# Kernel optimization log

Measured on AMD Instinct MI355X. Metric: run time of the kernel, lower is better.

Reference implementation:

```python
import jax, jax.numpy as jnp
import numpy as np

K = 3  # n_neighbors


def setup_inputs() -> dict:
    key = jax.random.key(0)
    k1, k2, k3 = jax.random.split(key, 3)
    N, D, C, B = 400000, 27, 11, 512  # train size, 3*N_PEAKS_MAX, classes, query batch
    train_features = jax.random.normal(k1, (N, D), dtype=jnp.float32)
    label_idx = jax.random.randint(k2, (N,), 0, C)
    train_labels = jax.nn.one_hot(label_idx, C, dtype=jnp.float32)
    query = jax.random.normal(k3, (B, D), dtype=jnp.float32)
    return {"query": query, "train_features": train_features, "train_labels": train_labels}


def _divide_no_nan(x, y):
    # tf.math.divide_no_nan: 0 where denominator is 0
    y_safe = jnp.where(y != 0, y, 1.0)
    return jnp.where(y != 0, x / y_safe, 0.0)


def reference(query, train_features, train_labels):
    # scale = per-feature max abs over training set (computed in __init__)
    scale = jnp.max(jnp.abs(train_features), axis=0)            # [D]
    train_s = _divide_no_nan(train_features, scale)             # [N,D]
    q_s = _divide_no_nan(query, scale)                          # [B,D]

    xn = jnp.sum(train_s * train_s, axis=1)                     # [N]
    qn = jnp.sum(q_s * q_s, axis=1)                             # [B]
    d2 = qn[:, None] - 2.0 * jnp.einsum('bd,nd->bn', q_s, train_s) + xn[None, :]
    dist = jnp.sqrt(jnp.maximum(d2, 0.0))                       # [B,N]

    neg_kd, idx = jax.lax.top_k(-dist, K)                       # k smallest distances
    kd = -neg_kd                                                # [B,K]

    lab = train_labels[idx]                                     # [B,K,C]
    # inverse-distance weighted vote (safe against zero distances)
    kd_safe = jnp.where(kd == 0.0, 1.0, kd)
    votes = jnp.sum(lab / kd_safe[:, :, None], axis=1)          # [B,C]
    vote_res = jax.nn.one_hot(jnp.argmax(votes, axis=1), train_labels.shape[1], dtype=jnp.float32)

    # exact-match branch: if the nearest distance is 0, return its label directly
    zero_hit = (jnp.min(kd, axis=1) == 0.0)[:, None]            # [B,1]
    result = jnp.where(zero_hit, lab[:, 0, :], vote_res)        # [B,C]
    return kd, result
```

## Files before the change

kernel.cpp:

```cpp
#include <hip/hip_runtime.h>
#include <math.h>

typedef _Float16 h8 __attribute__((ext_vector_type(8)));
typedef float    f4v __attribute__((ext_vector_type(4)));

#define N_TRAIN 400000
#define DIMS    27
#define BQ      512
#define NCLS    11
#define KNN     3
#define NB      500
#define P1T     1024
#define PTS_BLK 800
#define PTS_SUP 160
#define NSUP    5
#define NPT     10
#define RAWF    4320
#define TILE_B  2048
#define NC      (NB * KNN)
#define SB      1024
#define RPB     392
#define SROWS   128
#define P2T     512

#define U64MAX 0xFFFFFFFFFFFFFFFFULL

__global__ __launch_bounds__(256) void k_scale(const float* __restrict__ train,
                                               unsigned* __restrict__ scale_u) {
    __shared__ float st[SROWS * DIMS];
    __shared__ float sp[243];
    int tid = threadIdx.x;
    int r0 = blockIdx.x * RPB;
    int r1 = min(r0 + RPB, N_TRAIN);
    int c  = tid % DIMS;
    int rr = tid / DIMS;
    float m = 0.f;
    for (int base = r0; base < r1; base += SROWS) {
        int cnt = min(SROWS, r1 - base);
        int tot4 = (cnt * DIMS) >> 2;
        const uint4* src4 = (const uint4*)(train + (size_t)base * DIMS);
        uint4* st4 = (uint4*)st;
        for (int i = tid; i < tot4; i += 256) st4[i] = src4[i];
        __syncthreads();
        if (tid < 243) {
            for (int r = rr; r < cnt; r += 9)
                m = fmaxf(m, fabsf(st[r * DIMS + c]));
        }
        __syncthreads();
    }
    if (tid < 243) sp[tid] = m;
    __syncthreads();
    if (tid < DIMS) {
        float v = 0.f;
#pragma unroll
        for (int g = 0; g < 9; ++g) v = fmaxf(v, sp[g * DIMS + tid]);
        atomicMax(&scale_u[tid], __float_as_uint(v));
    }
}

__global__ __launch_bounds__(64) void k_qprep(const float* __restrict__ query,
                                              const unsigned* __restrict__ scale_u,
                                              _Float16* __restrict__ Qhi,
                                              _Float16* __restrict__ Qlo) {
    int q = blockIdx.x * 64 + threadIdx.x;
    if (q >= BQ) return;
    const float* r = query + (size_t)q * DIMS;
#pragma unroll
    for (int d = 0; d < 32; ++d) {
        _Float16 hi = (_Float16)0.f, lo = (_Float16)0.f;
        if (d < DIMS) {
            float sc = __uint_as_float(scale_u[d]);
            float inv = (sc != 0.f) ? 1.f / sc : 0.f;
            float xs = r[d] * inv;
            hi = (_Float16)xs;
            lo = (_Float16)(xs - (float)hi);
        } else if (d == 27) {
            hi = (_Float16)1.f;
        }
        Qhi[q * 32 + d] = hi;
        Qlo[q * 32 + d] = lo;
    }
}

__device__ __forceinline__ void insert3(float d, int i, float* bd, int* bi) {
    if (d < bd[2] || (d == bd[2] && i < bi[2])) {
        if (d < bd[1] || (d == bd[1] && i < bi[1])) {
            bd[2] = bd[1]; bi[2] = bi[1];
            if (d < bd[0] || (d == bd[0] && i < bi[0])) {
                bd[1] = bd[0]; bi[1] = bi[0];
                bd[0] = d; bi[0] = i;
            } else { bd[1] = d; bi[1] = i; }
        } else { bd[2] = d; bi[2] = i; }
    }
}

__device__ __forceinline__ unsigned long long shfl_xor_u64(unsigned long long v, int m) {
    unsigned lo = (unsigned)v, hi = (unsigned)(v >> 32);
    lo = __shfl_xor(lo, m, 64);
    hi = __shfl_xor(hi, m, 64);
    return ((unsigned long long)hi << 32) | lo;
}

__device__ __forceinline__ void ins3u64(unsigned long long e,
                                        unsigned long long& t0,
                                        unsigned long long& t1,
                                        unsigned long long& t2) {
    unsigned long long a  = e < t2 ? e : t2;
    unsigned long long n2 = t1 > a ? t1 : a;
    unsigned long long n1 = t1 < a ? t1 : a;
    t2 = n2;
    unsigned long long m1 = t0 > n1 ? t0 : n1;
    t0 = t0 < n1 ? t0 : n1;
    t1 = m1;
}

__device__ __forceinline__ void stage16(const float* g, float* l) {
    __builtin_amdgcn_global_load_lds((const __attribute__((address_space(1))) void*)g,
                                     (__attribute__((address_space(3))) void*)l, 16, 0, 0);
}

__global__ __attribute__((amdgpu_flat_work_group_size(P1T, P1T)))
__attribute__((amdgpu_waves_per_eu(4)))
void k_pass1(const float* __restrict__ train,
             const unsigned* __restrict__ scale_u,
             const _Float16* __restrict__ Qhi,
             const _Float16* __restrict__ Qlo,
             unsigned long long* __restrict__ cand) {
    __shared__ float s_inv[32];
    __shared__ __align__(16) float raw[2][RAWF];
    __shared__ __align__(16) unsigned char convb[2][NPT * TILE_B];

    int tid = threadIdx.x;
    if (tid < 32) {
        float sc = __uint_as_float(scale_u[tid]);
        s_inv[tid] = (sc != 0.f) ? 1.f / sc : 0.f;
    }
    int lane = tid & 63, w = tid >> 6;
    int l15 = lane & 15, quad = lane >> 4;

    h8 bhi[2], blo[2];
#pragma unroll
    for (int j = 0; j < 2; ++j) {
        int qt = w * 2 + j;
        size_t e = (size_t)(qt * 16 + l15) * 32 + quad * 8;
        bhi[j] = *(const h8*)(Qhi + e);
        blo[j] = *(const h8*)(Qlo + e);
    }

    unsigned kb0[2][4], kb1[2][4];
#pragma unroll
    for (int j = 0; j < 2; ++j)
#pragma unroll
        for (int r = 0; r < 4; ++r) { kb0[j][r] = 0u; kb1[j][r] = 0u; }

    const f4v z4 = {64.f, 64.f, 64.f, 64.f};

    int p0 = blockIdx.x * PTS_BLK;
    const float* gsup = train + (size_t)p0 * DIMS;

    {
        const float* gp = gsup; float* lp = raw[0];
        stage16(gp + tid * 4, lp + tid * 4);
        if (tid < 56) stage16(gp + 4096 + tid * 4, lp + 4096 + tid * 4);
    }

    for (int s = 0; s < NSUP; ++s) {
        __syncthreads();

        if (s + 1 < NSUP) {
            const float* gp = gsup + (size_t)(s + 1) * RAWF;
            float* lp = raw[(s + 1) & 1];
            stage16(gp + tid * 4, lp + tid * 4);
            if (tid < 56) stage16(gp + 4096 + tid * 4, lp + 4096 + tid * 4);
        }

        const float* rw = raw[s & 1];
        if (tid < PTS_SUP * 4) {
            int p = tid >> 2, gq = tid & 3;
            float x[8]; float part = 0.f;
#pragma unroll
            for (int i = 0; i < 8; ++i) {
                int d = gq * 8 + i;
                int dc = d < DIMS ? d : (DIMS - 1);
                float v = rw[p * DIMS + dc] * s_inv[d];
                x[i] = v;
                part = fmaf(v, v, part);
            }
            part += __shfl_xor(part, 1, 64);
            part += __shfl_xor(part, 2, 64);
            h8 hv, lv;
#pragma unroll
            for (int i = 0; i < 8; ++i) {
                _Float16 h = (_Float16)x[i];
                hv[i] = h;
                lv[i] = (_Float16)(x[i] - (float)h);
            }
            if (gq == 3) {
                float tt = -0.5f * part;
                _Float16 th = (_Float16)tt;
                hv[3] = th;
                lv[3] = (_Float16)(tt - (float)th);
            }
            unsigned char* dstb = convb[s & 1] + (p >> 4) * TILE_B + gq * 256 + (p & 15) * 16;
            *(h8*)dstb = hv;
            *(h8*)(dstb + 1024) = lv;
        }

        if (s > 0) {
            int ss = s - 1;
            const unsigned char* cb = convb[ss & 1];
            for (int t = 0; t < NPT; ++t) {
                const unsigned char* basep = cb + t * TILE_B;
                h8 ahi = *(const h8*)(basep + lane * 16);
                h8 alo = *(const h8*)(basep + 1024 + lane * 16);
                unsigned ic = 63u - (unsigned)(ss * NPT + t);
#pragma unroll
                for (int j = 0; j < 2; ++j) {
                    f4v acc;
                    acc = __builtin_amdgcn_mfma_f32_16x16x32_f16(alo, bhi[j], z4, 0, 0, 0);
                    acc = __builtin_amdgcn_mfma_f32_16x16x32_f16(ahi, blo[j], acc, 0, 0, 0);
                    acc = __builtin_amdgcn_mfma_f32_16x16x32_f16(ahi, bhi[j], acc, 0, 0, 0);
#pragma unroll
                    for (int r = 0; r < 4; ++r) {
                        unsigned key = (__float_as_uint(acc[r]) & 0xFFFFFFC0u) | ic;
                        unsigned b0 = kb0[j][r];
                        unsigned m  = key < b0 ? key : b0;
                        kb0[j][r]   = key > b0 ? key : b0;
                        unsigned b1 = kb1[j][r];
                        kb1[j][r]   = m > b1 ? m : b1;
                    }
                }
            }
        }
    }

    __syncthreads();
    {
        int ss = NSUP - 1;
        const unsigned char* cb = convb[ss & 1];
        for (int t = 0; t < NPT; ++t) {
            const unsigned char* basep = cb + t * TILE_B;
            h8 ahi = *(const h8*)(basep + lane * 16);
            h8 alo = *(const h8*)(basep + 1024 + lane * 16);
            unsigned ic = 63u - (unsigned)(ss * NPT + t);
#pragma unroll
            for (int j = 0; j < 2; ++j) {
                f4v acc;
                acc = __builtin_amdgcn_mfma_f32_16x16x32_f16(alo, bhi[j], z4, 0, 0, 0);
                acc = __builtin_amdgcn_mfma_f32_16x16x32_f16(ahi, blo[j], acc, 0, 0, 0);
                acc = __builtin_amdgcn_mfma_f32_16x16x32_f16(ahi, bhi[j], acc, 0, 0, 0);
#pragma unroll
                for (int r = 0; r < 4; ++r) {
                    unsigned key = (__float_as_uint(acc[r]) & 0xFFFFFFC0u) | ic;
                    unsigned b0 = kb0[j][r];
                    unsigned m  = key < b0 ? key : b0;
                    kb0[j][r]   = key > b0 ? key : b0;
                    unsigned b1 = kb1[j][r];
                    kb1[j][r]   = m > b1 ? m : b1;
                }
            }
        }
    }

    int g = blockIdx.x;
    int qr4 = quad * 4;
#pragma unroll
    for (int j = 0; j < 2; ++j) {
        unsigned long long t0 = U64MAX, t1 = U64MAX, t2 = U64MAX;
#pragma unroll
        for (int r = 0; r < 4; ++r) {
#pragma unroll
            for (int h = 0; h < 2; ++h) {
                unsigned k = h ? kb1[j][r] : kb0[j][r];
                unsigned tile = 63u - (k & 63u);
                unsigned gi = (unsigned)(p0 + (int)tile * 16 + qr4 + r);
                unsigned long long e = ((unsigned long long)(~(k | 63u)) << 32) | gi;
                ins3u64(e, t0, t1, t2);
            }
        }
#pragma unroll
        for (int step = 16; step <= 32; step <<= 1) {
            unsigned long long o0 = shfl_xor_u64(t0, step);
            unsigned long long o1 = shfl_xor_u64(t1, step);
            unsigned long long o2 = shfl_xor_u64(t2, step);
            ins3u64(o0, t0, t1, t2);
            ins3u64(o1, t0, t1, t2);
            ins3u64(o2, t0, t1, t2);
        }
        if (quad == 0) {
            int qq = (w * 2 + j) * 16 + l15;
            size_t off = (size_t)qq * NC + (size_t)g * KNN;
            cand[off + 0] = t0; cand[off + 1] = t1; cand[off + 2] = t2;
        }
    }
}

#define CE(a, b) do { unsigned long long lo_ = (a) < (b) ? (a) : (b); \
                      unsigned long long hi_ = (a) < (b) ? (b) : (a); \
                      (a) = lo_; (b) = hi_; } while (0)

__global__ __launch_bounds__(P2T) void k_pass2(const unsigned long long* __restrict__ cand,
                                               const float* __restrict__ train,
                                               const float* __restrict__ query,
                                               const unsigned* __restrict__ scale_u,
                                               const float* __restrict__ labels,
                                               float* __restrict__ out) {
    __shared__ unsigned long long smerge[64];
    int q = blockIdx.x;
    int tid = threadIdx.x, lane = tid & 63, w = tid >> 6;
    const unsigned long long* cd = cand + (size_t)q * NC;

    unsigned long long c0 = cd[tid];
    unsigned long long c1 = cd[tid + P2T];
    unsigned long long c2 = (tid + 2 * P2T < NC) ? cd[tid + 2 * P2T] : U64MAX;
    CE(c0, c1); CE(c0, c2); CE(c1, c2);

#pragma unroll
    for (int k = 0; k < 8; ++k) {
        unsigned long long m = c0;
#pragma unroll
        for (int st = 1; st < 64; st <<= 1) {
            unsigned long long o = shfl_xor_u64(m, st);
            if (o < m) m = o;
        }
        if (lane == 0) smerge[w * 8 + k] = m;
        bool win = (c0 == m);
        c0 = win ? c1 : c0;
        c1 = win ? c2 : c1;
        c2 = win ? U64MAX : c2;
    }
    __syncthreads();
    if (w != 0) return;

    int myi = 0x7fffffff;
    {
        unsigned long long cur = smerge[lane];
#pragma unroll
        for (int k = 0; k < 8; ++k) {
            unsigned long long m = cur;
#pragma unroll
            for (int st = 1; st < 64; st <<= 1) {
                unsigned long long o = shfl_xor_u64(m, st);
                if (o < m) m = o;
            }
            if (lane == k) myi = (int)(unsigned)m;
            if (cur == m) cur = U64MAX;
        }
    }

    float inv[DIMS], qs_[DIMS], qn_ = 0.f;
#pragma unroll
    for (int d = 0; d < DIMS; ++d) {
        float sc = __uint_as_float(scale_u[d]);
        float iv = (sc != 0.f) ? 1.f / sc : 0.f;
        float v = query[(size_t)q * DIMS + d] * iv;
        inv[d] = iv; qs_[d] = v;
        qn_ = fmaf(v, v, qn_);
    }

    float myd2 = 3.4e38f;
    if (lane < 8) {
        const float* r = train + (size_t)myi * DIMS;
        float xnv = 0.f, dot = 0.f;
#pragma unroll
        for (int d = 0; d < DIMS; ++d) {
            float v = r[d] * inv[d];
            xnv = fmaf(v, v, xnv);
            dot = fmaf(qs_[d], v, dot);
        }
        myd2 = fmaf(-2.f, dot, qn_ + xnv);
    }

    float bd[KNN] = {3.4e38f, 3.4e38f, 3.4e38f};
    int   bi[KNN] = {0x7fffffff, 0x7fffffff, 0x7fffffff};
#pragma unroll
    for (int k = 0; k < 8; ++k) {
        float dk = __shfl(myd2, k, 64);
        int   ik = __shfl(myi, k, 64);
        insert3(dk, ik, bd, bi);
    }

    if (lane == 0) {
        float kd[KNN];
#pragma unroll
        for (int k = 0; k < KNN; ++k) kd[k] = sqrtf(fmaxf(bd[k], 0.f));
        float lab[KNN][NCLS];
#pragma unroll
        for (int k = 0; k < KNN; ++k) {
            const float* lr = labels + (size_t)bi[k] * NCLS;
#pragma unroll
            for (int c = 0; c < NCLS; ++c) lab[k][c] = lr[c];
        }
        float votes[NCLS];
#pragma unroll
        for (int c = 0; c < NCLS; ++c) votes[c] = 0.f;
#pragma unroll
        for (int k = 0; k < KNN; ++k) {
            float ks = (kd[k] == 0.f) ? 1.f : kd[k];
#pragma unroll
            for (int c = 0; c < NCLS; ++c) votes[c] += lab[k][c] / ks;
        }
        int best = 0; float bv = votes[0];
#pragma unroll
        for (int c = 1; c < NCLS; ++c) { if (votes[c] > bv) { bv = votes[c]; best = c; } }
        bool zero_hit = (kd[0] == 0.f);
#pragma unroll
        for (int k = 0; k < KNN; ++k) out[(size_t)q * KNN + k] = kd[k];
        float* ro = out + (size_t)BQ * KNN + (size_t)q * NCLS;
#pragma unroll
        for (int c = 0; c < NCLS; ++c)
            ro[c] = zero_hit ? lab[0][c] : ((c == best) ? 1.f : 0.f);
    }
}

extern "C" void kernel_launch(void* const* d_in, const int* in_sizes, int n_in,
                              void* d_out, int out_size, void* d_ws, size_t ws_size,
                              hipStream_t stream) {
    const float* query  = (const float*)d_in[0];
    const float* train  = (const float*)d_in[1];
    const float* labels = (const float*)d_in[2];
    float* out = (float*)d_out;

    char* ws = (char*)d_ws;
    unsigned*  scale_u = (unsigned*)ws;
    _Float16*  Qhi = (_Float16*)(ws + 128);
    _Float16*  Qlo = (_Float16*)(ws + 32896);
    unsigned long long* cand = (unsigned long long*)(ws + 65664);

    hipMemsetAsync(ws, 0, 128, stream);
    k_scale<<<SB, 256, 0, stream>>>(train, scale_u);
    k_qprep<<<8, 64, 0, stream>>>(query, scale_u, Qhi, Qlo);
    k_pass1<<<NB, P1T, 0, stream>>>(train, scale_u, Qhi, Qlo, cand);
    k_pass2<<<BQ, P2T, 0, stream>>>(cand, train, query, scale_u, labels, out);
}
```

Measured before the change: 175.9 us.

## Fuse query prep into pass1 and rewrite scale reduction as register/shuffle max

```diff
diff --git a/kernel.cpp b/kernel.cpp
--- a/kernel.cpp
+++ b/kernel.cpp
@@ -18,67 +18,46 @@
 #define RAWF    4320
 #define TILE_B  2048
 #define NC      (NB * KNN)
-#define SB      1024
-#define RPB     392
-#define SROWS   128
+#define SCB     391
 #define P2T     512
 
 #define U64MAX 0xFFFFFFFFFFFFFFFFULL
 
 __global__ __launch_bounds__(256) void k_scale(const float* __restrict__ train,
                                                unsigned* __restrict__ scale_u) {
-    __shared__ float st[SROWS * DIMS];
-    __shared__ float sp[243];
+    __shared__ float red[4][DIMS];
     int tid = threadIdx.x;
-    int r0 = blockIdx.x * RPB;
-    int r1 = min(r0 + RPB, N_TRAIN);
-    int c  = tid % DIMS;
-    int rr = tid / DIMS;
-    float m = 0.f;
-    for (int base = r0; base < r1; base += SROWS) {
-        int cnt = min(SROWS, r1 - base);
-        int tot4 = (cnt * DIMS) >> 2;
-        const uint4* src4 = (const uint4*)(train + (size_t)base * DIMS);
-        uint4* st4 = (uint4*)st;
-        for (int i = tid; i < tot4; i += 256) st4[i] = src4[i];
-        __syncthreads();
-        if (tid < 243) {
-            for (int r = rr; r < cnt; r += 9)
-                m = fmaxf(m, fabsf(st[r * DIMS + c]));
-        }
-        __syncthreads();
-    }
-    if (tid < 243) sp[tid] = m;
+    int lane = tid & 63, w = tid >> 6;
+    int g = blockIdx.x * 256 + tid;
+    float m[DIMS];
+#pragma unroll
+    for (int d = 0; d < DIMS; ++d) m[d] = 0.f;
+    if (g < N_TRAIN / 4) {
+        const uint4* p = (const uint4*)(train + (size_t)g * (4 * DIMS));
+#pragma unroll
+        for (int k = 0; k < DIMS; ++k) {
+            uint4 v = p[k];
+            m[(4 * k + 0) % DIMS] = fmaxf(m[(4 * k + 0) % DIMS], fabsf(__uint_as_float(v.x)));
+            m[(4 * k + 1) % DIMS] = fmaxf(m[(4 * k + 1) % DIMS], fabsf(__uint_as_float(v.y)));
+            m[(4 * k + 2) % DIMS] = fmaxf(m[(4 * k + 2) % DIMS], fabsf(__uint_as_float(v.z)));
+            m[(4 * k + 3) % DIMS] = fmaxf(m[(4 * k + 3) % DIMS], fabsf(__uint_as_float(v.w)));
+        }
+    }
+#pragma unroll
+    for (int d = 0; d < DIMS; ++d) {
+        float t = m[d];
+#pragma unroll
+        for (int st = 1; st < 64; st <<= 1) t = fmaxf(t, __shfl_xor(t, st, 64));
+        m[d] = t;
+    }
+    if (lane == 0) {
+#pragma unroll
+        for (int d = 0; d < DIMS; ++d) red[w][d] = m[d];
+    }
     __syncthreads();
     if (tid < DIMS) {
-        float v = 0.f;
-#pragma unroll
-        for (int g = 0; g < 9; ++g) v = fmaxf(v, sp[g * DIMS + tid]);
+        float v = fmaxf(fmaxf(red[0][tid], red[1][tid]), fmaxf(red[2][tid], red[3][tid]));
         atomicMax(&scale_u[tid], __float_as_uint(v));
-    }
-}
-
-__global__ __launch_bounds__(64) void k_qprep(const float* __restrict__ query,
-                                              const unsigned* __restrict__ scale_u,
-                                              _Float16* __restrict__ Qhi,
-                                              _Float16* __restrict__ Qlo) {
-    int q = blockIdx.x * 64 + threadIdx.x;
-    if (q >= BQ) return;
-    const float* r = query + (size_t)q * DIMS;
-#pragma unroll
-    for (int d = 0; d < 32; ++d) {
-        _Float16 hi = (_Float16)0.f, lo = (_Float16)0.f;
-        if (d < DIMS) {
-            float sc = __uint_as_float(scale_u[d]);
-            float inv = (sc != 0.f) ? 1.f / sc : 0.f;
-            float xs = r[d] * inv;
-            hi = (_Float16)xs;
-            lo = (_Float16)(xs - (float)hi);
-        } else if (d == 27) {
-            hi = (_Float16)1.f;
-        }
-        Qhi[q * 32 + d] = hi;
-        Qlo[q * 32 + d] = lo;
     }
 }
 
@@ -123,8 +102,7 @@
 __attribute__((amdgpu_waves_per_eu(4)))
 void k_pass1(const float* __restrict__ train,
              const unsigned* __restrict__ scale_u,
-             const _Float16* __restrict__ Qhi,
-             const _Float16* __restrict__ Qlo,
+             const float* __restrict__ query,
              unsigned long long* __restrict__ cand) {
     __shared__ float s_inv[32];
     __shared__ __align__(16) float raw[2][RAWF];
@@ -138,23 +116,6 @@
     int lane = tid & 63, w = tid >> 6;
     int l15 = lane & 15, quad = lane >> 4;
 
-    h8 bhi[2], blo[2];
-#pragma unroll
-    for (int j = 0; j < 2; ++j) {
-        int qt = w * 2 + j;
-        size_t e = (size_t)(qt * 16 + l15) * 32 + quad * 8;
-        bhi[j] = *(const h8*)(Qhi + e);
-        blo[j] = *(const h8*)(Qlo + e);
-    }
-
-    unsigned kb0[2][4], kb1[2][4];
-#pragma unroll
-    for (int j = 0; j < 2; ++j)
-#pragma unroll
-        for (int r = 0; r < 4; ++r) { kb0[j][r] = 0u; kb1[j][r] = 0u; }
-
-    const f4v z4 = {64.f, 64.f, 64.f, 64.f};
-
     int p0 = blockIdx.x * PTS_BLK;
     const float* gsup = train + (size_t)p0 * DIMS;
 
@@ -163,6 +124,39 @@
         stage16(gp + tid * 4, lp + tid * 4);
         if (tid < 56) stage16(gp + 4096 + tid * 4, lp + 4096 + tid * 4);
     }
+
+    float iv_[8];
+#pragma unroll
+    for (int i = 0; i < 8; ++i) {
+        int d = quad * 8 + i;
+        float sc = __uint_as_float(scale_u[d]);
+        iv_[i] = (sc != 0.f) ? 1.f / sc : 0.f;
+    }
+    h8 bhi[2], blo[2];
+#pragma unroll
+    for (int j = 0; j < 2; ++j) {
+        int q = (w * 2 + j) * 16 + l15;
+        const float* qr = query + (size_t)q * DIMS;
+#pragma unroll
+        for (int i = 0; i < 8; ++i) {
+            int d = quad * 8 + i;
+            int dc = d < DIMS ? d : (DIMS - 1);
+            float xs = qr[dc] * iv_[i];
+            _Float16 hi = (_Float16)xs;
+            _Float16 lo = (_Float16)(xs - (float)hi);
+            bool is27 = (d == 27);
+            bhi[j][i] = is27 ? (_Float16)1.f : hi;
+            blo[j][i] = is27 ? (_Float16)0.f : lo;
+        }
+    }
+
+    unsigned kb0[2][4], kb1[2][4];
+#pragma unroll
+    for (int j = 0; j < 2; ++j)
+#pragma unroll
+        for (int r = 0; r < 4; ++r) { kb0[j][r] = 0u; kb1[j][r] = 0u; }
+
+    const f4v z4 = {64.f, 64.f, 64.f, 64.f};
 
     for (int s = 0; s < NSUP; ++s) {
         __syncthreads();
@@ -423,13 +417,10 @@
 
     char* ws = (char*)d_ws;
     unsigned*  scale_u = (unsigned*)ws;
-    _Float16*  Qhi = (_Float16*)(ws + 128);
-    _Float16*  Qlo = (_Float16*)(ws + 32896);
-    unsigned long long* cand = (unsigned long long*)(ws + 65664);
+    unsigned long long* cand = (unsigned long long*)(ws + 128);
 
     hipMemsetAsync(ws, 0, 128, stream);
-    k_scale<<<SB, 256, 0, stream>>>(train, scale_u);
-    k_qprep<<<8, 64, 0, stream>>>(query, scale_u, Qhi, Qlo);
-    k_pass1<<<NB, P1T, 0, stream>>>(train, scale_u, Qhi, Qlo, cand);
+    k_scale<<<SCB, 256, 0, stream>>>(train, scale_u);
+    k_pass1<<<NB, P1T, 0, stream>>>(train, scale_u, query, cand);
     k_pass2<<<BQ, P2T, 0, stream>>>(cand, train, query, scale_u, labels, out);
 }
```

New measurement: 176.8 us. About the same (+0.5%).
